# Performance work log

Hardware: AMD Instinct MI355X
Metric: run time of the kernel (lower is better)

The kernel has to match this reference:

```python
import jax, jax.numpy as jnp
import numpy as np

B, S, D, H, E, K = 4, 2048, 1024, 4096, 8, 2
CAP_RATIO = 1.05


def setup_inputs() -> dict:
    key = jax.random.key(0)
    k0, k1, k2, k3 = jax.random.split(key, 4)
    x = jax.random.normal(k0, (B, S, D), jnp.float32)
    # router gating weight (xavier-uniform-ish scale)
    Wg = jax.random.normal(k1, (E, D), jnp.float32) * np.float32(np.sqrt(2.0 / (D + E)))
    W1 = jax.random.normal(k2, (E, D, H), jnp.float32) * np.float32(0.02)
    b1 = jnp.zeros((E, H), jnp.float32)
    W2 = jax.random.normal(k3, (E, H, D), jnp.float32) * np.float32(0.02)
    b2 = jnp.zeros((E, D), jnp.float32)
    return {"x": x, "Wg": Wg, "W1": W1, "b1": b1, "W2": W2, "b2": b2}


def reference(x, Wg, W1, b1, W2, b2):
    Bs, Ss, Dd = x.shape
    T = Bs * Ss
    C = int(round(K * T * CAP_RATIO / E))  # static buffer capacity per expert
    xf = x.reshape(T, Dd)

    # --- router (eval mode: no noise) ---
    logits = xf @ Wg.T                       # (T, E)
    gates = jax.nn.softmax(logits, axis=-1)  # (T, E)
    topv, topi = jax.lax.top_k(gates, K)     # (T, K)

    # --- capacity-limited dispatch: FCFS over slot-major (slot, token) order ---
    idx_sm = topi.T.reshape(-1)                              # (K*T,) slot-major expert ids
    oh = jax.nn.one_hot(idx_sm, E, dtype=jnp.int32)          # (K*T, E)
    pos_sm = (jnp.cumsum(oh, axis=0) * oh).sum(-1) - 1       # 0-based rank within expert
    within_sm = pos_sm < C
    pos_sm = jnp.where(within_sm, pos_sm, C)                 # C == out-of-bounds sentinel
    pos = pos_sm.reshape(K, T).T                             # (T, K)
    within = within_sm.reshape(K, T).T                       # (T, K) bool

    # --- combine weights: mask dropped slots, renormalize over active slots ---
    w = topv * within.astype(topv.dtype)
    sums = w.sum(-1, keepdims=True)
    w = jnp.where(sums > 0, w / sums, w)

    # --- scatter tokens into per-expert capacity buffers ---
    e_flat = topi.reshape(-1)                                # (T*K,)
    pos_flat = pos.reshape(-1)                               # (T*K,)
    x_ts = jnp.broadcast_to(xf[:, None, :], (T, K, Dd)).reshape(T * K, Dd)
    expert_in = jnp.zeros((E, C, Dd), x.dtype).at[e_flat, pos_flat].set(x_ts, mode='drop')

    # --- per-expert MLP (grouped GEMM) ---
    h = jax.nn.gelu(jnp.einsum('ecd,edh->ech', expert_in, W1) + b1[:, None, :], approximate=False)
    o = jnp.einsum('ech,ehd->ecd', h, W2) + b2[:, None, :]   # (E, C, D)

    # --- gather back and weighted combine (dropped slots gather 0) ---
    y_ts = o.at[e_flat, pos_flat].get(mode='fill', fill_value=0).reshape(T, K, Dd)
    y = jnp.einsum('tk,tkd->td', w, y_ts)                    # (T, D)

    # --- auxiliary losses ---
    imp = gates.sum(0)                                       # (E,)
    l_imp = (jnp.std(imp) / (imp.mean() + 1e-6)) ** 2
    tpe = (oh * within_sm[:, None].astype(jnp.int32)).sum(0).astype(jnp.float32)
    l_load = (jnp.std(tpe) / (tpe.mean() + 1e-6)) ** 2
    l_aux = 0.5 * (l_imp + l_load)

    return y.reshape(Bs, Ss, Dd), l_aux, l_load
```

## Files before the change

### kernel.cpp

```cpp
#include <hip/hip_runtime.h>
#include <math.h>

typedef short short8v __attribute__((ext_vector_type(8)));
typedef float f32x4 __attribute__((ext_vector_type(4)));
typedef unsigned short ushort4v __attribute__((ext_vector_type(4)));

#define T_TOK 8192
#define DDIM 1024
#define HDIM 4096
#define NE 8
#define CCAP 2150
#define CPAD 2304

__device__ __forceinline__ unsigned short f2bf(float f) {
  union { float f; unsigned u; } a; a.f = f;
  unsigned r = a.u + 0x7fffu + ((a.u >> 16) & 1u);
  return (unsigned short)(r >> 16);
}
__device__ __forceinline__ float bf2f(unsigned short h) {
  union { unsigned u; float f; } a; a.u = ((unsigned)h) << 16;
  return a.f;
}

#define GLOAD_LDS16(gp, lp)                                                   \
  __builtin_amdgcn_global_load_lds(                                           \
      (const __attribute__((address_space(1))) void*)(gp),                    \
      (__attribute__((address_space(3))) void*)(lp), 16, 0, 0)

#define BAR()                                   \
  do {                                          \
    asm volatile("" ::: "memory");              \
    __builtin_amdgcn_s_barrier();               \
    asm volatile("" ::: "memory");              \
  } while (0)

__global__ __launch_bounds__(256) void router_kernel(
    const float* __restrict__ x, const float* __restrict__ Wg,
    int2* __restrict__ topi, float2* __restrict__ topv,
    float* __restrict__ blkimp) {
  __shared__ float wg[NE * DDIM];
  __shared__ float gsh[4][NE];
  int tid = threadIdx.x;
  for (int i = tid; i < NE * DDIM / 4; i += 256)
    ((float4*)wg)[i] = ((const float4*)Wg)[i];
  __syncthreads();
  int w = tid >> 6, lane = tid & 63;
  int t = blockIdx.x * 4 + w;
  const float* xr = x + (size_t)t * DDIM;
  float p[NE] = {0.f, 0.f, 0.f, 0.f, 0.f, 0.f, 0.f, 0.f};
#pragma unroll
  for (int j = 0; j < 16; ++j) {
    float xv = xr[lane + 64 * j];
#pragma unroll
    for (int e = 0; e < NE; ++e)
      p[e] = fmaf(xv, wg[e * DDIM + lane + 64 * j], p[e]);
  }
#pragma unroll
  for (int e = 0; e < NE; ++e) {
#pragma unroll
    for (int off = 32; off > 0; off >>= 1) p[e] += __shfl_xor(p[e], off, 64);
  }
  float mx = p[0];
#pragma unroll
  for (int e = 1; e < NE; ++e) mx = fmaxf(mx, p[e]);
  float g[NE];
  float s = 0.f;
#pragma unroll
  for (int e = 0; e < NE; ++e) { g[e] = expf(p[e] - mx); s += g[e]; }
  float inv = 1.0f / s;
#pragma unroll
  for (int e = 0; e < NE; ++e) g[e] *= inv;
  int i0 = 0; float v0 = g[0];
#pragma unroll
  for (int e = 1; e < NE; ++e) if (g[e] > v0) { v0 = g[e]; i0 = e; }
  int i1 = -1; float v1 = -1.0f;
#pragma unroll
  for (int e = 0; e < NE; ++e)
    if (e != i0 && g[e] > v1) { v1 = g[e]; i1 = e; }
  if (lane == 0) {
    topi[t] = make_int2(i0, i1);
    topv[t] = make_float2(v0, v1);
#pragma unroll
    for (int e = 0; e < NE; ++e) gsh[w][e] = g[e];
  }
  __syncthreads();
  if (tid < NE)
    blkimp[blockIdx.x * NE + tid] =
        gsh[0][tid] + gsh[1][tid] + gsh[2][tid] + gsh[3][tid];
}

__global__ __launch_bounds__(256) void dispatch_kernel(
    const int2* __restrict__ topi, const float2* __restrict__ topv,
    const float* __restrict__ blkimp, int2* __restrict__ posmj,
    float2* __restrict__ wmaj, float* __restrict__ tail) {
  __shared__ unsigned char eid[2 * T_TOK];
  __shared__ unsigned short possm[2 * T_TOK];
  __shared__ int cnt_sh[NE];
  __shared__ float part[32][NE];
  int tid = threadIdx.x;
  for (int i = tid; i < T_TOK; i += 256) {
    int2 ti = topi[i];
    eid[i] = (unsigned char)ti.x;
    eid[T_TOK + i] = (unsigned char)ti.y;
  }
  __syncthreads();
  if (tid < 64) {
    int lane = tid;
    unsigned long long low = (1ull << lane) - 1ull;
    int c0 = 0, c1 = 0, c2 = 0, c3 = 0, c4 = 0, c5 = 0, c6 = 0, c7 = 0;
    for (int base = 0; base < 2 * T_TOK; base += 64) {
      int e = eid[base + lane];
      unsigned long long m0 = __ballot(e == 0);
      unsigned long long m1 = __ballot(e == 1);
      unsigned long long m2 = __ballot(e == 2);
      unsigned long long m3 = __ballot(e == 3);
      unsigned long long m4 = __ballot(e == 4);
      unsigned long long m5 = __ballot(e == 5);
      unsigned long long m6 = __ballot(e == 6);
      unsigned long long m7 = __ballot(e == 7);
      int rank = 0;
      if (e == 0) rank = c0 + __popcll(m0 & low);
      if (e == 1) rank = c1 + __popcll(m1 & low);
      if (e == 2) rank = c2 + __popcll(m2 & low);
      if (e == 3) rank = c3 + __popcll(m3 & low);
      if (e == 4) rank = c4 + __popcll(m4 & low);
      if (e == 5) rank = c5 + __popcll(m5 & low);
      if (e == 6) rank = c6 + __popcll(m6 & low);
      if (e == 7) rank = c7 + __popcll(m7 & low);
      possm[base + lane] = (unsigned short)((rank < CCAP) ? rank : CCAP);
      c0 += __popcll(m0); c1 += __popcll(m1); c2 += __popcll(m2);
      c3 += __popcll(m3); c4 += __popcll(m4); c5 += __popcll(m5);
      c6 += __popcll(m6); c7 += __popcll(m7);
    }
    if (lane == 0) {
      cnt_sh[0] = c0; cnt_sh[1] = c1; cnt_sh[2] = c2; cnt_sh[3] = c3;
      cnt_sh[4] = c4; cnt_sh[5] = c5; cnt_sh[6] = c6; cnt_sh[7] = c7;
    }
  }
  __syncthreads();
  for (int t = tid; t < T_TOK; t += 256) {
    int p0 = possm[t], p1 = possm[T_TOK + t];
    float2 tv = topv[t];
    float w0 = (p0 < CCAP) ? tv.x : 0.0f;
    float w1 = (p1 < CCAP) ? tv.y : 0.0f;
    float s = w0 + w1;
    if (s > 0.0f) { w0 /= s; w1 /= s; }
    posmj[t] = make_int2(p0, p1);
    wmaj[t] = make_float2(w0, w1);
  }
  {
    int sl = tid >> 3, e8 = tid & 7;
    float s = 0.f;
    for (int b = sl; b < 2048; b += 32) s += blkimp[b * NE + e8];
    part[sl][e8] = s;
  }
  __syncthreads();
  if (tid == 0) {
    float imp[NE], te[NE];
    for (int e = 0; e < NE; ++e) {
      float s = 0.f;
      for (int j = 0; j < 32; ++j) s += part[j][e];
      imp[e] = s;
      int c = cnt_sh[e];
      te[e] = (float)(c < CCAP ? c : CCAP);
    }
    float mi = 0.f, mt = 0.f;
    for (int e = 0; e < NE; ++e) { mi += imp[e]; mt += te[e]; }
    mi *= 0.125f; mt *= 0.125f;
    float vi = 0.f, vt = 0.f;
    for (int e = 0; e < NE; ++e) {
      vi += (imp[e] - mi) * (imp[e] - mi);
      vt += (te[e] - mt) * (te[e] - mt);
    }
    vi *= 0.125f; vt *= 0.125f;
    float ai = sqrtf(vi) / (mi + 1e-6f);
    float at = sqrtf(vt) / (mt + 1e-6f);
    tail[0] = 0.5f * (ai * ai + at * at);
    tail[1] = at * at;
  }
}

__global__ __launch_bounds__(256) void scatter_kernel(
    const float* __restrict__ x, const int2* __restrict__ topi,
    const int2* __restrict__ posmj, unsigned short* __restrict__ ein) {
  int tid = threadIdx.x;
  int gid = blockIdx.x * 4 + (tid >> 6);
  int lane = tid & 63;
  int t = gid >> 1, k = gid & 1;
  int2 pp = posmj[t];
  int p = k ? pp.y : pp.x;
  if (p >= CCAP) return;
  int2 ii = topi[t];
  int e = k ? ii.y : ii.x;
  const float4* src = (const float4*)(x + (size_t)t * DDIM);
  unsigned short* dst = ein + ((size_t)e * CPAD + p) * DDIM;
#pragma unroll
  for (int j = 0; j < 4; ++j) {
    int c = j * 64 + lane;
    float4 v = src[c];
    ushort4v o;
    o.x = f2bf(v.x); o.y = f2bf(v.y); o.z = f2bf(v.z); o.w = f2bf(v.w);
    *(ushort4v*)(dst + (size_t)c * 4) = o;
  }
}

__global__ __launch_bounds__(256) void transpose_cvt_kernel(
    const float* __restrict__ W, unsigned short* __restrict__ WT, int R,
    int Cc) {
  __shared__ unsigned short tile[64][72];
  int rt = R >> 6, ct = Cc >> 6;
  int per_e = rt * ct;
  int e = blockIdx.x / per_e;
  int rem = blockIdx.x % per_e;
  int tr = rem % rt, tc = rem / rt;
  int r0 = tr << 6, c0 = tc << 6;
  const float* We = W + (size_t)e * R * Cc;
  unsigned short* WTe = WT + (size_t)e * R * Cc;
  int tid = threadIdx.x;
  {
    int rl = tid >> 2, cb = (tid & 3) << 4;
    const float* src = We + (size_t)(r0 + rl) * Cc + c0 + cb;
#pragma unroll
    for (int j = 0; j < 16; j += 4) {
      float4 v = *(const float4*)(src + j);
      tile[rl][cb + j + 0] = f2bf(v.x);
      tile[rl][cb + j + 1] = f2bf(v.y);
      tile[rl][cb + j + 2] = f2bf(v.z);
      tile[rl][cb + j + 3] = f2bf(v.w);
    }
  }
  __syncthreads();
  {
    int cl = tid >> 2, rb = (tid & 3) << 4;
    unsigned short* dst = WTe + (size_t)(c0 + cl) * R + r0 + rb;
#pragma unroll
    for (int j = 0; j < 16; j += 4) {
      ushort4v o;
      o.x = tile[rb + j + 0][cl];
      o.y = tile[rb + j + 1][cl];
      o.z = tile[rb + j + 2][cl];
      o.w = tile[rb + j + 3][cl];
      *(ushort4v*)(dst + j) = o;
    }
  }
}

template <bool GELU>
__global__ __launch_bounds__(512, 2) void gemm256_kernel(
    const unsigned short* __restrict__ A, const unsigned short* __restrict__ B,
    const float* __restrict__ bias, unsigned short* __restrict__ Out0,
    unsigned short* __restrict__ Out1, int M, int N, int Kz, int Ksub, int NT,
    int mt, int nt) {
  __shared__ __align__(16) char smem[131072];
  int nwg = gridDim.x;
  int bid = blockIdx.x;
  int swz = (bid & 7) * (nwg >> 3) + (bid >> 3);
  int bm = swz % mt;
  int r = swz / mt;
  int bn = r % nt;
  int r2 = r / nt;
  int e = r2 & 7;
  int ks = r2 >> 3;
  unsigned short* Outp = ks ? Out1 : Out0;
  int koff = ks * Ksub;

  int tid = threadIdx.x;
  int w = tid >> 6, lane = tid & 63;
  int wm = w >> 2, wn = w & 3;
  int fr = lane & 15, g = lane >> 4;
  size_t Kzs = (size_t)Kz;
  const char* Ab = (const char*)(A + ((size_t)e * M + (size_t)bm * 256) * Kzs + koff);
  const char* Bb = (const char*)(B + ((size_t)e * N + (size_t)bn * 256) * Kzs + koff);

  size_t ro0 = (size_t)(w * 16 + fr) * Kzs * 2 + (size_t)g * 16;
  size_t ro1 = ro0 + (size_t)128 * Kzs * 2;
  int ld0 = (w << 10) + lane * 16;
  int ld1 = ((8 + w) << 10) + lane * 16;

  auto stage = [&](const char* gb, int buf, int isB, int kh) {
    int base = (isB << 16) + (buf << 15) + (kh << 14);
    GLOAD_LDS16(gb + ro0 + kh * 64, smem + base + ld0);
    GLOAD_LDS16(gb + ro1 + kh * 64, smem + base + ld1);
  };
  auto lda = [&](int buf, int kk, int m16) -> short8v {
    return *(const short8v*)(smem + (buf << 15) + (kk << 14) + (m16 << 10) +
                             lane * 16);
  };
  auto ldb = [&](int buf, int kk, int n16) -> short8v {
    return *(const short8v*)(smem + 65536 + (buf << 15) + (kk << 14) +
                             (n16 << 10) + lane * 16);
  };

  f32x4 acc[8][4] = {};
  short8v a0[4], a1[4], b0[4], b1[4];

  stage(Ab, 0, 0, 0); stage(Bb, 0, 1, 0);
  stage(Ab, 0, 0, 1); stage(Bb, 0, 1, 1);
  stage(Ab + 128, 1, 0, 0); stage(Bb + 128, 1, 1, 0);
  asm volatile("s_waitcnt vmcnt(8)" ::: "memory");
  BAR();
#pragma unroll
  for (int m = 0; m < 4; ++m) a0[m] = lda(0, 0, wm * 8 + m);
#pragma unroll
  for (int n = 0; n < 4; ++n) b0[n] = ldb(0, 0, wn * 4 + n);

  for (int t = 0; t < NT; ++t) {
    int c = t & 1, cn = c ^ 1;
    const char* At1 = Ab + (size_t)(t + 1) * 128;
    const char* Bt1 = Bb + (size_t)(t + 1) * 128;
    const char* At2 = Ab + (size_t)(t + 2) * 128;
    const char* Bt2 = Bb + (size_t)(t + 2) * 128;
#pragma unroll
    for (int m = 0; m < 4; ++m) a1[m] = lda(c, 0, wm * 8 + 4 + m);
    if (t + 1 < NT) stage(At1, cn, 0, 1);
    BAR();
    __builtin_amdgcn_s_setprio(1);
#pragma unroll
    for (int m = 0; m < 4; ++m)
#pragma unroll
      for (int n = 0; n < 4; ++n)
        acc[m][n] = __builtin_amdgcn_mfma_f32_16x16x32_bf16(a0[m], b0[n],
                                                            acc[m][n], 0, 0, 0);
    __builtin_amdgcn_s_setprio(0);
    if (t + 1 < NT) {
      asm volatile("s_waitcnt vmcnt(6)" ::: "memory");
    } else {
      asm volatile("s_waitcnt vmcnt(0)" ::: "memory");
    }
    BAR();
#pragma unroll
    for (int m = 0; m < 4; ++m) a0[m] = lda(c, 1, wm * 8 + m);
#pragma unroll
    for (int n = 0; n < 4; ++n) b1[n] = ldb(c, 1, wn * 4 + n);
    if (t + 1 < NT) stage(Bt1, cn, 1, 1);
    BAR();
    __builtin_amdgcn_s_setprio(1);
#pragma unroll
    for (int m = 0; m < 4; ++m)
#pragma unroll
      for (int n = 0; n < 4; ++n)
        acc[4 + m][n] = __builtin_amdgcn_mfma_f32_16x16x32_bf16(
            a1[m], b0[n], acc[4 + m][n], 0, 0, 0);
    __builtin_amdgcn_s_setprio(0);
    BAR();
#pragma unroll
    for (int m = 0; m < 4; ++m) a1[m] = lda(c, 1, wm * 8 + 4 + m);
    if (t + 2 < NT) stage(At2, c, 0, 0);
    BAR();
    __builtin_amdgcn_s_setprio(1);
#pragma unroll
    for (int m = 0; m < 4; ++m)
#pragma unroll
      for (int n = 0; n < 4; ++n)
        acc[m][n] = __builtin_amdgcn_mfma_f32_16x16x32_bf16(a0[m], b1[n],
                                                            acc[m][n], 0, 0, 0);
    __builtin_amdgcn_s_setprio(0);
    BAR();
    if (t + 2 < NT) {
      stage(Bt2, c, 1, 0);
      asm volatile("s_waitcnt vmcnt(8)" ::: "memory");
    } else if (t + 1 < NT) {
      asm volatile("s_waitcnt vmcnt(4)" ::: "memory");
    } else {
      asm volatile("s_waitcnt vmcnt(0)" ::: "memory");
    }
    BAR();
    if (t + 1 < NT) {
#pragma unroll
      for (int m = 0; m < 4; ++m) a0[m] = lda(cn, 0, wm * 8 + m);
#pragma unroll
      for (int n = 0; n < 4; ++n) b0[n] = ldb(cn, 0, wn * 4 + n);
    }
    __builtin_amdgcn_s_setprio(1);
#pragma unroll
    for (int m = 0; m < 4; ++m)
#pragma unroll
      for (int n = 0; n < 4; ++n)
        acc[4 + m][n] = __builtin_amdgcn_mfma_f32_16x16x32_bf16(
            a1[m], b1[n], acc[4 + m][n], 0, 0, 0);
    __builtin_amdgcn_s_setprio(0);
    BAR();
  }

  float bv[4];
#pragma unroll
  for (int n = 0; n < 4; ++n)
    bv[n] = (ks == 0)
                ? bias[(size_t)e * N + (size_t)bn * 256 + wn * 64 + n * 16 + fr]
                : 0.0f;
  char* wreg = smem + w * 16384;
#pragma unroll
  for (int m = 0; m < 8; ++m)
#pragma unroll
    for (int n = 0; n < 4; ++n)
#pragma unroll
      for (int j = 0; j < 4; ++j) {
        float v = acc[m][n][j] + bv[n];
        if (GELU) v = 0.5f * v * (1.0f + erff(v * 0.70710678118654752f));
        int rl = m * 16 + g * 4 + j;
        *(unsigned short*)(wreg + rl * 128 + (n * 16 + fr) * 2) = f2bf(v);
      }
  unsigned short* Oe = Outp +
                       ((size_t)e * M + (size_t)bm * 256 + (size_t)wm * 128) * N +
                       (size_t)bn * 256 + (size_t)wn * 64;
#pragma unroll
  for (int pass = 0; pass < 16; ++pass) {
    int rr = pass * 8 + (lane >> 3);
    int ch = lane & 7;
    short8v vv = *(const short8v*)(wreg + rr * 128 + ch * 16);
    *(short8v*)(Oe + (size_t)rr * N + ch * 8) = vv;
  }
}

__global__ __launch_bounds__(256) void gather_kernel(
    const unsigned short* __restrict__ obufA,
    const unsigned short* __restrict__ obufB, const int2* __restrict__ topi,
    const int2* __restrict__ posmj, const float2* __restrict__ wmaj,
    float* __restrict__ y) {
  int tid = threadIdx.x;
  int w = tid >> 6, lane = tid & 63;
  int t = blockIdx.x * 4 + w;
  int2 pp = posmj[t];
  int2 ii = topi[t];
  float2 ww = wmaj[t];
  float* yr = y + (size_t)t * DDIM;
  size_t o0 = ((size_t)ii.x * CPAD + pp.x) * DDIM;
  size_t o1 = ((size_t)ii.y * CPAD + pp.y) * DDIM;
  bool v0 = pp.x < CCAP, v1 = pp.y < CCAP;
#pragma unroll
  for (int j = 0; j < 4; ++j) {
    int c = j * 64 + lane;
    float ax = 0.f, ay = 0.f, az = 0.f, aw = 0.f;
    if (v0) {
      ushort4v a = *(const ushort4v*)(obufA + o0 + (size_t)c * 4);
      ushort4v b = *(const ushort4v*)(obufB + o0 + (size_t)c * 4);
      ax += ww.x * (bf2f(a.x) + bf2f(b.x));
      ay += ww.x * (bf2f(a.y) + bf2f(b.y));
      az += ww.x * (bf2f(a.z) + bf2f(b.z));
      aw += ww.x * (bf2f(a.w) + bf2f(b.w));
    }
    if (v1) {
      ushort4v a = *(const ushort4v*)(obufA + o1 + (size_t)c * 4);
      ushort4v b = *(const ushort4v*)(obufB + o1 + (size_t)c * 4);
      ax += ww.y * (bf2f(a.x) + bf2f(b.x));
      ay += ww.y * (bf2f(a.y) + bf2f(b.y));
      az += ww.y * (bf2f(a.z) + bf2f(b.z));
      aw += ww.y * (bf2f(a.w) + bf2f(b.w));
    }
    ((float4*)yr)[c] = make_float4(ax, ay, az, aw);
  }
}

extern "C" void kernel_launch(void* const* d_in, const int* in_sizes, int n_in,
                              void* d_out, int out_size, void* d_ws,
                              size_t ws_size, hipStream_t stream) {
  (void)in_sizes; (void)n_in; (void)out_size; (void)ws_size;
  const float* x = (const float*)d_in[0];
  const float* Wg = (const float*)d_in[1];
  const float* W1 = (const float*)d_in[2];
  const float* b1 = (const float*)d_in[3];
  const float* W2 = (const float*)d_in[4];
  const float* b2 = (const float*)d_in[5];
  float* out = (float*)d_out;

  char* ws = (char*)d_ws;
  size_t off = 0;
  auto alloc = [&](size_t b) {
    char* p = ws + off;
    off += (b + 255) & ~(size_t)255;
    return p;
  };
  unsigned short* ein = (unsigned short*)alloc((size_t)NE * CPAD * DDIM * 2);
  unsigned short* hbuf = (unsigned short*)alloc((size_t)NE * CPAD * HDIM * 2);
  unsigned short* obuf = (unsigned short*)alloc((size_t)NE * CPAD * DDIM * 2);
  unsigned short* w1t = (unsigned short*)alloc((size_t)NE * HDIM * DDIM * 2);
  unsigned short* w2t = (unsigned short*)alloc((size_t)NE * DDIM * HDIM * 2);
  int2* topi = (int2*)alloc(T_TOK * sizeof(int2));
  float2* topv = (float2*)alloc(T_TOK * sizeof(float2));
  int2* posmj = (int2*)alloc(T_TOK * sizeof(int2));
  float2* wmaj = (float2*)alloc(T_TOK * sizeof(float2));
  float* blkimp = (float*)alloc(2048 * NE * sizeof(float));

  transpose_cvt_kernel<<<NE * (DDIM / 64) * (HDIM / 64), 256, 0, stream>>>(
      W1, w1t, DDIM, HDIM);
  transpose_cvt_kernel<<<NE * (HDIM / 64) * (DDIM / 64), 256, 0, stream>>>(
      W2, w2t, HDIM, DDIM);
  router_kernel<<<T_TOK / 4, 256, 0, stream>>>(x, Wg, topi, topv, blkimp);
  dispatch_kernel<<<1, 256, 0, stream>>>(topi, topv, blkimp, posmj, wmaj,
                                         out + (size_t)T_TOK * DDIM);
  scatter_kernel<<<(2 * T_TOK) / 4, 256, 0, stream>>>(x, topi, posmj, ein);

  gemm256_kernel<true><<<NE * 9 * 16, 512, 0, stream>>>(
      ein, w1t, b1, hbuf, hbuf, CPAD, HDIM, DDIM, DDIM, DDIM / 64, 9, 16);
  gemm256_kernel<false><<<NE * 9 * 4 * 2, 512, 0, stream>>>(
      hbuf, w2t, b2, obuf, ein, CPAD, DDIM, HDIM, HDIM / 2, HDIM / 128, 9, 4);

  gather_kernel<<<T_TOK / 4, 256, 0, stream>>>(obuf, ein, topi, posmj, wmaj,
                                               out);
}
```

Baseline: 680.9 us.

## Restructure GEMM main loop with inline-asm LDS reads and explicit waitcnt scheduling

Replaces the C++ LDS fragment loads with inline ds_read_b128 asm on precomputed LDS addresses, and reorganizes the K-loop so each quarter-step loads its A/B fragments, waits on lgkmcnt(0) and issues a 16-MFMA block behind sched_barriers. The register double-buffering of fragments (a0/a1/b0/b1) is dropped for a single Af/Bk set, which cuts register pressure, and the vmcnt wait points move. It also removes the memory clobbers around the barriers to give the compiler more scheduling freedom. In exchange, LDS reads no longer overlap the previous MFMA block, so latency may be exposed, and the hand-placed waits carry correctness risk.

Result: no change. 677.4 us (-0.5%).

```diff
diff --git a/kernel.cpp b/kernel.cpp
--- a/kernel.cpp
+++ b/kernel.cpp
@@ -27,11 +27,17 @@
       (const __attribute__((address_space(1))) void*)(gp),                    \
       (__attribute__((address_space(3))) void*)(lp), 16, 0, 0)
 
-#define BAR()                                   \
-  do {                                          \
-    asm volatile("" ::: "memory");              \
-    __builtin_amdgcn_s_barrier();               \
-    asm volatile("" ::: "memory");              \
+__device__ __forceinline__ short8v ds_read128(unsigned addr) {
+  short8v v;
+  asm volatile("ds_read_b128 %0, %1" : "=v"(v) : "v"(addr));
+  return v;
+}
+
+#define BAR() __builtin_amdgcn_s_barrier()
+#define WLGKM0()                                  \
+  do {                                            \
+    asm volatile("s_waitcnt lgkmcnt(0)");         \
+    __builtin_amdgcn_sched_barrier(0);            \
   } while (0)
 
 __global__ __launch_bounds__(256) void router_kernel(
@@ -282,105 +288,83 @@
     GLOAD_LDS16(gb + ro0 + kh * 64, smem + base + ld0);
     GLOAD_LDS16(gb + ro1 + kh * 64, smem + base + ld1);
   };
-  auto lda = [&](int buf, int kk, int m16) -> short8v {
-    return *(const short8v*)(smem + (buf << 15) + (kk << 14) + (m16 << 10) +
-                             lane * 16);
-  };
-  auto ldb = [&](int buf, int kk, int n16) -> short8v {
-    return *(const short8v*)(smem + 65536 + (buf << 15) + (kk << 14) +
-                             (n16 << 10) + lane * 16);
-  };
+
+  unsigned sbase =
+      (unsigned)(unsigned long long)(__attribute__((address_space(3))) char*)smem;
+  unsigned l16 = (unsigned)(lane * 16);
+  unsigned am = sbase + (unsigned)((wm * 8) << 10) + l16;
+  unsigned bnr = sbase + 65536u + (unsigned)((wn * 4) << 10) + l16;
 
   f32x4 acc[8][4] = {};
-  short8v a0[4], a1[4], b0[4], b1[4];
+  short8v Af[4], Bk[4];
+
+#define MM16(RO)                                                           \
+  do {                                                                     \
+    __builtin_amdgcn_s_setprio(1);                                         \
+    _Pragma("unroll") for (int m_ = 0; m_ < 4; ++m_)                       \
+        _Pragma("unroll") for (int n_ = 0; n_ < 4; ++n_)                   \
+            acc[RO + m_][n_] = __builtin_amdgcn_mfma_f32_16x16x32_bf16(    \
+                Af[m_], Bk[n_], acc[RO + m_][n_], 0, 0, 0);                \
+    __builtin_amdgcn_s_setprio(0);                                         \
+    __builtin_amdgcn_sched_barrier(0);                                     \
+  } while (0)
 
   stage(Ab, 0, 0, 0); stage(Bb, 0, 1, 0);
   stage(Ab, 0, 0, 1); stage(Bb, 0, 1, 1);
   stage(Ab + 128, 1, 0, 0); stage(Bb + 128, 1, 1, 0);
-  asm volatile("s_waitcnt vmcnt(8)" ::: "memory");
+  asm volatile("s_waitcnt vmcnt(8)");
   BAR();
-#pragma unroll
-  for (int m = 0; m < 4; ++m) a0[m] = lda(0, 0, wm * 8 + m);
-#pragma unroll
-  for (int n = 0; n < 4; ++n) b0[n] = ldb(0, 0, wn * 4 + n);
 
   for (int t = 0; t < NT; ++t) {
     int c = t & 1, cn = c ^ 1;
+    unsigned cb = (unsigned)(c << 15);
     const char* At1 = Ab + (size_t)(t + 1) * 128;
     const char* Bt1 = Bb + (size_t)(t + 1) * 128;
     const char* At2 = Ab + (size_t)(t + 2) * 128;
     const char* Bt2 = Bb + (size_t)(t + 2) * 128;
 #pragma unroll
-    for (int m = 0; m < 4; ++m) a1[m] = lda(c, 0, wm * 8 + 4 + m);
+    for (int n = 0; n < 4; ++n) Bk[n] = ds_read128(bnr + cb + (n << 10));
+#pragma unroll
+    for (int m = 0; m < 4; ++m) Af[m] = ds_read128(am + cb + (m << 10));
     if (t + 1 < NT) stage(At1, cn, 0, 1);
     BAR();
-    __builtin_amdgcn_s_setprio(1);
+    WLGKM0();
+    MM16(0);
+    BAR();
 #pragma unroll
     for (int m = 0; m < 4; ++m)
-#pragma unroll
-      for (int n = 0; n < 4; ++n)
-        acc[m][n] = __builtin_amdgcn_mfma_f32_16x16x32_bf16(a0[m], b0[n],
-                                                            acc[m][n], 0, 0, 0);
-    __builtin_amdgcn_s_setprio(0);
-    if (t + 1 < NT) {
-      asm volatile("s_waitcnt vmcnt(6)" ::: "memory");
-    } else {
-      asm volatile("s_waitcnt vmcnt(0)" ::: "memory");
-    }
-    BAR();
-#pragma unroll
-    for (int m = 0; m < 4; ++m) a0[m] = lda(c, 1, wm * 8 + m);
-#pragma unroll
-    for (int n = 0; n < 4; ++n) b1[n] = ldb(c, 1, wn * 4 + n);
+      Af[m] = ds_read128(am + cb + ((4 + m) << 10));
     if (t + 1 < NT) stage(Bt1, cn, 1, 1);
     BAR();
-    __builtin_amdgcn_s_setprio(1);
+    WLGKM0();
+    MM16(4);
+    if (t + 1 < NT) asm volatile("s_waitcnt vmcnt(8)");
+    else            asm volatile("s_waitcnt vmcnt(0)");
+    BAR();
+#pragma unroll
+    for (int n = 0; n < 4; ++n)
+      Bk[n] = ds_read128(bnr + cb + 16384u + (n << 10));
 #pragma unroll
     for (int m = 0; m < 4; ++m)
-#pragma unroll
-      for (int n = 0; n < 4; ++n)
-        acc[4 + m][n] = __builtin_amdgcn_mfma_f32_16x16x32_bf16(
-            a1[m], b0[n], acc[4 + m][n], 0, 0, 0);
-    __builtin_amdgcn_s_setprio(0);
-    BAR();
-#pragma unroll
-    for (int m = 0; m < 4; ++m) a1[m] = lda(c, 1, wm * 8 + 4 + m);
+      Af[m] = ds_read128(am + cb + 16384u + (m << 10));
     if (t + 2 < NT) stage(At2, c, 0, 0);
     BAR();
-    __builtin_amdgcn_s_setprio(1);
+    WLGKM0();
+    MM16(0);
+    BAR();
 #pragma unroll
     for (int m = 0; m < 4; ++m)
-#pragma unroll
-      for (int n = 0; n < 4; ++n)
-        acc[m][n] = __builtin_amdgcn_mfma_f32_16x16x32_bf16(a0[m], b1[n],
-                                                            acc[m][n], 0, 0, 0);
-    __builtin_amdgcn_s_setprio(0);
-    BAR();
-    if (t + 2 < NT) {
-      stage(Bt2, c, 1, 0);
-      asm volatile("s_waitcnt vmcnt(8)" ::: "memory");
-    } else if (t + 1 < NT) {
-      asm volatile("s_waitcnt vmcnt(4)" ::: "memory");
-    } else {
-      asm volatile("s_waitcnt vmcnt(0)" ::: "memory");
-    }
-    BAR();
-    if (t + 1 < NT) {
-#pragma unroll
-      for (int m = 0; m < 4; ++m) a0[m] = lda(cn, 0, wm * 8 + m);
-#pragma unroll
-      for (int n = 0; n < 4; ++n) b0[n] = ldb(cn, 0, wn * 4 + n);
-    }
-    __builtin_amdgcn_s_setprio(1);
-#pragma unroll
-    for (int m = 0; m < 4; ++m)
-#pragma unroll
-      for (int n = 0; n < 4; ++n)
-        acc[4 + m][n] = __builtin_amdgcn_mfma_f32_16x16x32_bf16(
-            a1[m], b1[n], acc[4 + m][n], 0, 0, 0);
-    __builtin_amdgcn_s_setprio(0);
-    BAR();
-  }
+      Af[m] = ds_read128(am + cb + 16384u + ((4 + m) << 10));
+    if (t + 2 < NT) stage(Bt2, c, 1, 0);
+    BAR();
+    WLGKM0();
+    MM16(4);
+    if (t + 2 < NT)      asm volatile("s_waitcnt vmcnt(8)");
+    else if (t + 1 < NT) asm volatile("s_waitcnt vmcnt(4)");
+    else                 asm volatile("s_waitcnt vmcnt(0)");
+    BAR();
+  }
+#undef MM16
 
   float bv[4];
 #pragma unroll
```
